# Kernel optimization log

Measured on AMD Instinct MI355X. Metric: run time of the kernel, lower is better.

## Reference

```python
import jax, jax.numpy as jnp
import numpy as np

N, E, F, H, C, T = 100000, 1600000, 128, 64, 8, 4

def setup_inputs() -> dict:
    key = jax.random.key(0)
    ks = jax.random.split(key, 16)
    inp = {
        'x': jax.random.normal(ks[0], (N, F), dtype=jnp.float32),
        'node_types': jax.random.randint(ks[1], (N,), 0, T, dtype=jnp.int64),
        'edge_index0': jax.random.randint(ks[2], (2, E), 0, N, dtype=jnp.int64),
        'edge_index1': jax.random.randint(ks[3], (2, E), 0, N, dtype=jnp.int64),
        # per-node-type input projections
        'W_in': jax.random.normal(ks[4], (T, F, H), dtype=jnp.float32) / np.sqrt(F),
        'b_in': jnp.zeros((T, H), dtype=jnp.float32),
        # 4 GCN convs (layer0: paths [0,0],[0,1]; layer1: paths [0,0],[1,0])
        'W_conv': jax.random.normal(ks[5], (4, H, H), dtype=jnp.float32) / np.sqrt(H),
        'b_conv': jnp.zeros((4, H), dtype=jnp.float32),
        # output attention/classifier layers
        'W1': jax.random.normal(ks[6], (H, H), dtype=jnp.float32) / np.sqrt(H),
        'b1': jnp.zeros((H,), dtype=jnp.float32),
        'W2': jax.random.normal(ks[7], (H, 1), dtype=jnp.float32) / np.sqrt(H),
        'b2': jnp.zeros((1,), dtype=jnp.float32),
        'W3': jax.random.normal(ks[8], (H, C), dtype=jnp.float32) / np.sqrt(H),
        'b3': jnp.zeros((C,), dtype=jnp.float32),
    }
    return inp


def gcn_conv(x, edge_index, W, b):
    # PyG GCNConv: add self-loops, symmetric normalization, then scatter-add.
    n = x.shape[0]
    loop = jnp.arange(n, dtype=edge_index.dtype)
    src = jnp.concatenate([edge_index[0], loop])
    dst = jnp.concatenate([edge_index[1], loop])
    deg = jax.ops.segment_sum(jnp.ones_like(dst, dtype=x.dtype), dst, num_segments=n)
    dinv = jnp.where(deg > 0, jax.lax.rsqrt(deg), 0.0)
    norm = dinv[src] * dinv[dst]            # [E+N]
    xw = x @ W                              # [N,H]
    msg = xw[src] * norm[:, None]           # [E+N,H]
    out = jax.ops.segment_sum(msg, dst, num_segments=n)
    return out + b


def reference(x, node_types, edge_index0, edge_index1,
              W_in, b_in, W_conv, b_conv, W1, b1, W2, b2, W3, b3):
    # per-node-type input linear (fixed small loop over T types)
    hid = jnp.zeros((x.shape[0], H), dtype=x.dtype)
    for t in range(T):
        ht = x @ W_in[t] + b_in[t]
        hid = jnp.where((node_types == t)[:, None], ht, hid)
    edges = [edge_index0, edge_index1]
    states = [hid]
    # layer 0: paths [state 0, adj 0], [state 0, adj 1]; layer_agg = max
    h0 = gcn_conv(states[0], edges[0], W_conv[0], b_conv[0])
    h1 = gcn_conv(states[0], edges[1], W_conv[1], b_conv[1])
    states.append(jnp.maximum(h0, h1))
    # layer 1: paths [state 0, adj 0], [state 1, adj 0]
    h2 = gcn_conv(states[0], edges[0], W_conv[2], b_conv[2])
    h3 = gcn_conv(states[1], edges[0], W_conv[3], b_conv[3])
    states.append(jnp.maximum(h2, h3))
    # LayerNorm (no affine) + gelu (torch default = exact erf form)
    tmp = states[-1]
    mu = jnp.mean(tmp, axis=-1, keepdims=True)
    var = jnp.mean(jnp.square(tmp - mu), axis=-1, keepdims=True)
    tmp = (tmp - mu) * jax.lax.rsqrt(var + 1e-5)
    hidi = jax.nn.gelu(tmp, approximate=False)
    # attention combine over (single) temp state
    attn = jax.nn.softmax(jnp.tanh(hidi @ W1 + b1) @ W2 + b2, axis=-1)  # [N,1] -> ones
    out = attn * hidi
    return out @ W3 + b3
```

## Files before the change

### kernel.cpp

```cpp
#include <hip/hip_runtime.h>
#include <hip/hip_bf16.h>
#include <math.h>


#define HID   64
#define RB    128
#define CHUNK 4096

__device__ __forceinline__ float bflo(unsigned u) { return __int_as_float((int)(u << 16)); }
__device__ __forceinline__ float bfhi(unsigned u) { return __int_as_float((int)(u & 0xFFFF0000u)); }
__device__ __forceinline__ float bf2f(ushort v) { return __int_as_float((int)(((unsigned)v) << 16)); }
__device__ __forceinline__ ushort f2bf(float f) {
    unsigned u = __float_as_uint(f);
    unsigned r = u + 0x7FFFu + ((u >> 16) & 1u);
    return (ushort)(r >> 16);
}

__global__ void zeroRow(unsigned* __restrict__ ghz, unsigned* __restrict__ s1z,
                        float* __restrict__ dinv0, float* __restrict__ dinv1, int N) {
    int tid = threadIdx.x;
    if (tid < 32) { ghz[tid] = 0u; s1z[tid] = 0u; }
    if (tid == 0) { dinv0[N] = 0.0f; dinv1[N] = 0.0f; }
}

__global__ void histA(const int* __restrict__ dst0, const int* __restrict__ dst1,
                      int E, unsigned M, int* __restrict__ bcnt) {
    __shared__ int h[2 * RB];
    for (int i = threadIdx.x; i < 2 * RB; i += blockDim.x) h[i] = 0;
    __syncthreads();
    int stride = gridDim.x * blockDim.x;
    for (int i = blockIdx.x * blockDim.x + threadIdx.x; i < E; i += stride) {
        atomicAdd(&h[__umulhi((unsigned)dst0[i], M)], 1);
        atomicAdd(&h[RB + __umulhi((unsigned)dst1[i], M)], 1);
    }
    __syncthreads();
    for (int i = threadIdx.x; i < 2 * RB; i += blockDim.x)
        if (h[i]) atomicAdd(&bcnt[i], h[i]);
}

__global__ void scanA(const int* __restrict__ bcnt, int* __restrict__ bbase,
                      int* __restrict__ bcur) {
    __shared__ int t[2 * RB];
    int tid = threadIdx.x;
    int orig = bcnt[tid];
    t[tid] = orig;
    __syncthreads();
    int list = tid >> 7, r = tid & (RB - 1);
    for (int o = 1; o < RB; o <<= 1) {
        int u = (r >= o) ? t[tid - o] : 0;
        __syncthreads();
        t[tid] += u;
        __syncthreads();
    }
    int incl = t[tid];
    int excl = incl - orig;
    bbase[list * (RB + 1) + r] = excl;
    bcur[tid] = excl;
    if (r == RB - 1) bbase[list * (RB + 1) + RB] = incl;
}

__global__ void __launch_bounds__(256) partB(const int* __restrict__ e0,
                                             const int* __restrict__ e1,
                                             int E, int BW, unsigned M,
                                             int* __restrict__ bcur_all,
                                             unsigned* __restrict__ arena_all) {
    __shared__ int hist[RB], scn[RB], lbase[RB], cur[RB], gbase[RB];
    __shared__ uint2 buf[CHUNK];
    int half = gridDim.x >> 1;
    int list = (blockIdx.x >= half) ? 1 : 0;
    const int* src = list ? e1 : e0;
    const int* dst = src + E;
    int* bcur = bcur_all + list * RB;
    unsigned* arena = arena_all + (size_t)list * E;
    int blk = blockIdx.x - list * half;
    int tid = threadIdx.x;

    for (int c0 = blk * CHUNK; c0 < E; c0 += half * CHUNK) {
        int cn = min(CHUNK, E - c0);
        for (int i = tid; i < RB; i += 256) hist[i] = 0;
        __syncthreads();
        unsigned ls[16], ld[16];
        #pragma unroll
        for (int k = 0; k < 16; ++k) {
            int j = k * 256 + tid;
            ld[k] = 0xFFFFFFFFu; ls[k] = 0;
            if (j < cn) {
                ls[k] = (unsigned)src[c0 + j];
                ld[k] = (unsigned)dst[c0 + j];
                atomicAdd(&hist[__umulhi(ld[k], M)], 1);
            }
        }
        __syncthreads();
        if (tid < RB) scn[tid] = hist[tid];
        __syncthreads();
        for (int o = 1; o < RB; o <<= 1) {
            int u = (tid < RB && tid >= o) ? scn[tid - o] : 0;
            __syncthreads();
            if (tid < RB) scn[tid] += u;
            __syncthreads();
        }
        if (tid < RB) {
            int ex = scn[tid] - hist[tid];
            lbase[tid] = ex;
            cur[tid]   = ex;
            gbase[tid] = hist[tid] ? atomicAdd(&bcur[tid], hist[tid]) : 0;
        }
        __syncthreads();
        #pragma unroll
        for (int k = 0; k < 16; ++k) {
            if (ld[k] != 0xFFFFFFFFu) {
                int b = __umulhi(ld[k], M);
                int slot = atomicAdd(&cur[b], 1);
                buf[slot] = make_uint2(ls[k], ld[k]);
            }
        }
        __syncthreads();
        for (int i = tid; i < cn; i += 256) {
            uint2 p = buf[i];
            int b = __umulhi(p.y, M);
            arena[gbase[b] + (i - lbase[b])] = (p.x << 10) | (p.y - (unsigned)(b * BW));
        }
        __syncthreads();
    }
}

__global__ void __launch_bounds__(1024) buildC(const unsigned* __restrict__ arena_all,
                                               const int* __restrict__ bbase,
                                               int E, int N, int BW,
                                               int* __restrict__ csr0p, int* __restrict__ csr1p,
                                               unsigned* __restrict__ offp0, unsigned* __restrict__ offp1,
                                               float* __restrict__ dinv0, float* __restrict__ dinv1) {
    __shared__ int degl[800], scn[800], cur[800];
    int list = blockIdx.x >> 7, rb = blockIdx.x & (RB - 1);
    const unsigned* arena = arena_all + (size_t)list * E;
    int* csr = list ? csr1p : csr0p;
    unsigned* offp = list ? offp1 : offp0;
    float* dinv = list ? dinv1 : dinv0;
    int base = bbase[list * (RB + 1) + rb];
    int end  = bbase[list * (RB + 1) + rb + 1];
    int csrb = base + 8 * BW * rb;
    int nbase = rb * BW;
    int nn = min(BW, N - nbase);
    if (nn <= 0) return;
    int tid = threadIdx.x;
    for (int i = tid; i < nn; i += 1024) degl[i] = 0;
    __syncthreads();
    for (int j = base + tid; j < end; j += 1024)
        atomicAdd(&degl[arena[j] & 1023u], 1);
    __syncthreads();
    int d = (tid < nn) ? degl[tid] : 0;
    int dp = d ? ((d + 7) & ~7) : 0;
    if (tid < nn) scn[tid] = dp;
    __syncthreads();
    for (int o = 1; o < nn; o <<= 1) {
        int u = (tid < nn && tid >= o) ? scn[tid - o] : 0;
        __syncthreads();
        if (tid < nn) scn[tid] += u;
        __syncthreads();
    }
    if (tid < nn) {
        int ex = scn[tid] - dp;
        cur[tid] = ex;
        offp[nbase + tid] = (unsigned)(csrb + ex) | ((unsigned)(dp >> 3) << 25);
        dinv[nbase + tid] = rsqrtf((float)(d + 1));
        for (int j = ex + d; j < ex + dp; ++j) csr[csrb + j] = N;
    }
    __syncthreads();
    for (int j = base + tid; j < end; j += 1024) {
        unsigned p = arena[j];
        int loc = atomicAdd(&cur[p & 1023u], 1);
        csr[csrb + loc] = (int)(p >> 10);
    }
}

__global__ void input_proj(const float* __restrict__ x, const int* __restrict__ types,
                           const float* __restrict__ W_in, const float* __restrict__ b_in,
                           ushort* __restrict__ gh, int N, int F) {
    __shared__ float xs[4 * 128];
    int tid = threadIdx.x;
    int w = tid >> 6, h = tid & 63;
    int n0 = blockIdx.x * 4;
    for (int i = tid; i < 4 * F; i += 256) {
        int nn = n0 + i / F;
        xs[i] = (nn < N) ? x[(size_t)nn * F + (i % F)] : 0.0f;
    }
    __syncthreads();
    int n = n0 + w;
    if (n >= N) return;
    int t = types[n];
    const float* W = W_in + (size_t)t * F * HID;
    float acc = b_in[t * HID + h];
    const float* xr = xs + w * F;
    #pragma unroll 4
    for (int f = 0; f < F; ++f)
        acc = fmaf(xr[f], W[(size_t)f * HID + h], acc);
    gh[(size_t)n * HID + h] = f2bf(acc);
}

__device__ __forceinline__ void gather_w(const uint2* __restrict__ GH,
                                         const float* __restrict__ dv,
                                         const int* __restrict__ csr,
                                         unsigned wword, int q, int fl, float a[4]) {
    int base = (int)(wword & 0x1FFFFFFu);
    int it = (int)(wword >> 25);
    if (it == 0) return;
    const int* cp = csr + base;
    int ia = cp[q], ib = cp[4 + q];
    while (true) {
        uint2 va = GH[(size_t)ia * 16 + fl];
        uint2 vb = GH[(size_t)ib * 16 + fl];
        float wa = dv[ia], wb = dv[ib];
        --it; cp += 8;
        int na = 0, nb = 0;
        if (it > 0) { na = cp[q]; nb = cp[4 + q]; }
        a[0] = fmaf(bflo(va.x), wa, a[0]);
        a[1] = fmaf(bfhi(va.x), wa, a[1]);
        a[2] = fmaf(bflo(va.y), wa, a[2]);
        a[3] = fmaf(bfhi(va.y), wa, a[3]);
        a[0] = fmaf(bflo(vb.x), wb, a[0]);
        a[1] = fmaf(bfhi(vb.x), wb, a[1]);
        a[2] = fmaf(bflo(vb.y), wb, a[2]);
        a[3] = fmaf(bfhi(vb.y), wb, a[3]);
        if (it == 0) break;
        ia = na; ib = nb;
    }
}

__device__ __forceinline__ void gather_u(const uint2* __restrict__ GH,
                                         const int* __restrict__ csr,
                                         unsigned wword, int q, int fl, float a[4]) {
    int base = (int)(wword & 0x1FFFFFFu);
    int it = (int)(wword >> 25);
    if (it == 0) return;
    const int* cp = csr + base;
    int ia = cp[q], ib = cp[4 + q];
    while (true) {
        uint2 va = GH[(size_t)ia * 16 + fl];
        uint2 vb = GH[(size_t)ib * 16 + fl];
        --it; cp += 8;
        int na = 0, nb = 0;
        if (it > 0) { na = cp[q]; nb = cp[4 + q]; }
        a[0] += bflo(va.x) + bflo(vb.x);
        a[1] += bfhi(va.x) + bfhi(vb.x);
        a[2] += bflo(va.y) + bflo(vb.y);
        a[3] += bfhi(va.y) + bfhi(vb.y);
        if (it == 0) break;
        ia = na; ib = nb;
    }
}

__global__ void __launch_bounds__(512) gatherL1(
        const ushort* __restrict__ gh,
        const unsigned* __restrict__ offp0, const int* __restrict__ csr0p,
        const float* __restrict__ dinv0,
        const unsigned* __restrict__ offp1, const int* __restrict__ csr1p,
        const float* __restrict__ dinv1,
        const float* __restrict__ W_conv, const float* __restrict__ b_conv,
        unsigned* __restrict__ a0g, ushort* __restrict__ s1g, int N) {
    __shared__ ushort Wb[2 * HID * HID];
    __shared__ float l0[8][HID], l1[8][HID];
    int tid = threadIdx.x;
    for (int i = tid; i < 2 * HID * HID; i += 512) Wb[i] = f2bf(W_conv[i]);
    __syncthreads();
    int w = tid >> 6, lane = tid & 63;
    int q = lane >> 4, fl = lane & 15;
    int n = blockIdx.x * 8 + w;
    if (n >= N) return;
    const uint2* GH = (const uint2*)gh;
    float d0 = dinv0[n], d1 = dinv1[n];
    float a0[4] = {0, 0, 0, 0}, a1[4] = {0, 0, 0, 0};
    if (q == 0) {
        uint2 sv = GH[(size_t)n * 16 + fl];
        a0[0] = bflo(sv.x) * d0; a0[1] = bfhi(sv.x) * d0;
        a0[2] = bflo(sv.y) * d0; a0[3] = bfhi(sv.y) * d0;
        a1[0] = bflo(sv.x) * d1; a1[1] = bfhi(sv.x) * d1;
        a1[2] = bflo(sv.y) * d1; a1[3] = bfhi(sv.y) * d1;
    }
    gather_w(GH, dinv0, csr0p, offp0[n], q, fl, a0);
    gather_w(GH, dinv1, csr1p, offp1[n], q, fl, a1);
    #pragma unroll
    for (int k = 0; k < 4; ++k) {
        a0[k] += __shfl_xor(a0[k], 16, 64);
        a0[k] += __shfl_xor(a0[k], 32, 64);
        a1[k] += __shfl_xor(a1[k], 16, 64);
        a1[k] += __shfl_xor(a1[k], 32, 64);
        a0[k] *= d0;
        a1[k] *= d1;
    }
    if (q == 0) {
        *(float4*)&l0[w][fl * 4] = make_float4(a0[0], a0[1], a0[2], a0[3]);
        *(float4*)&l1[w][fl * 4] = make_float4(a1[0], a1[1], a1[2], a1[3]);
        uint2 pk;
        pk.x = (unsigned)f2bf(a0[0]) | ((unsigned)f2bf(a0[1]) << 16);
        pk.y = (unsigned)f2bf(a0[2]) | ((unsigned)f2bf(a0[3]) << 16);
        ((uint2*)a0g)[(size_t)n * 16 + fl] = pk;
    }
    int h = lane;
    float m0 = b_conv[h];
    float m1 = b_conv[HID + h];
    #pragma unroll 8
    for (int k = 0; k < HID; ++k) {
        m0 = fmaf(l0[w][k], bf2f(Wb[k * HID + h]), m0);
        m1 = fmaf(l1[w][k], bf2f(Wb[HID * HID + k * HID + h]), m1);
    }
    s1g[(size_t)n * HID + h] = f2bf(fmaxf(m0, m1) * d0);
}

__global__ void __launch_bounds__(512) gatherL2(
        const unsigned* __restrict__ a0g, const ushort* __restrict__ s1g,
        const unsigned* __restrict__ offp0, const int* __restrict__ csr0p,
        const float* __restrict__ dinv0,
        const float* __restrict__ W_conv, const float* __restrict__ b_conv,
        const float* __restrict__ W3, const float* __restrict__ b3,
        float* __restrict__ out, int N) {
    __shared__ ushort Wb[2 * HID * HID];
    __shared__ float W3s[HID * 8];
    __shared__ float l2[8][HID], l3[8][HID], gs[8][HID];
    int tid = threadIdx.x;
    for (int i = tid; i < 2 * HID * HID; i += 512) Wb[i] = f2bf(W_conv[2 * HID * HID + i]);
    if (tid < HID * 8) W3s[tid] = W3[tid];
    __syncthreads();
    int w = tid >> 6, lane = tid & 63;
    int q = lane >> 4, fl = lane & 15;
    int n = blockIdx.x * 8 + w;
    if (n >= N) return;
    const uint2* S = (const uint2*)s1g;
    float d0 = dinv0[n];
    float a[4] = {0, 0, 0, 0};
    if (q == 0) {
        uint2 sv = S[(size_t)n * 16 + fl];
        a[0] = bflo(sv.x); a[1] = bfhi(sv.x);
        a[2] = bflo(sv.y); a[3] = bfhi(sv.y);
        uint2 av = ((const uint2*)a0g)[(size_t)n * 16 + fl];
        *(float4*)&l2[w][fl * 4] = make_float4(bflo(av.x), bfhi(av.x), bflo(av.y), bfhi(av.y));
    }
    gather_u(S, csr0p, offp0[n], q, fl, a);
    #pragma unroll
    for (int k = 0; k < 4; ++k) {
        a[k] += __shfl_xor(a[k], 16, 64);
        a[k] += __shfl_xor(a[k], 32, 64);
        a[k] *= d0;
    }
    if (q == 0)
        *(float4*)&l3[w][fl * 4] = make_float4(a[0], a[1], a[2], a[3]);
    int h = lane;
    float m2 = b_conv[2 * HID + h];
    float m3 = b_conv[3 * HID + h];
    #pragma unroll 8
    for (int k = 0; k < HID; ++k) {
        m2 = fmaf(l2[w][k], bf2f(Wb[k * HID + h]), m2);
        m3 = fmaf(l3[w][k], bf2f(Wb[HID * HID + k * HID + h]), m3);
    }
    float s2 = fmaxf(m2, m3);
    float sum = s2;
    #pragma unroll
    for (int off = 32; off; off >>= 1) sum += __shfl_xor(sum, off, 64);
    float mu = sum * (1.0f / 64.0f);
    float dv = s2 - mu;
    float v = dv * dv;
    #pragma unroll
    for (int off = 32; off; off >>= 1) v += __shfl_xor(v, off, 64);
    float xn = dv * rsqrtf(v * (1.0f / 64.0f) + 1e-5f);
    float g = 0.5f * xn * (1.0f + erff(xn * 0.70710678118654752f));
    gs[w][h] = g;
    if (h < 8) {
        float acc = b3[h];
        #pragma unroll 8
        for (int k = 0; k < HID; ++k)
            acc = fmaf(gs[w][k], W3s[k * 8 + h], acc);
        out[(size_t)n * 8 + h] = acc;
    }
}

extern "C" void kernel_launch(void* const* d_in, const int* in_sizes, int n_in,
                              void* d_out, int out_size, void* d_ws, size_t ws_size,
                              hipStream_t stream) {
    const float* x          = (const float*)d_in[0];
    const int*   node_types = (const int*)d_in[1];
    const int*   e0         = (const int*)d_in[2];
    const int*   e1         = (const int*)d_in[3];
    const float* W_in       = (const float*)d_in[4];
    const float* b_in       = (const float*)d_in[5];
    const float* W_conv     = (const float*)d_in[6];
    const float* b_conv     = (const float*)d_in[7];
    const float* W3         = (const float*)d_in[12];
    const float* b3         = (const float*)d_in[13];
    float* out = (float*)d_out;

    int N = in_sizes[1];
    int F = in_sizes[0] / N;
    int E = in_sizes[2] / 2;
    int BW = (N + RB - 1) / RB;
    unsigned M = (unsigned)(0x100000000ULL / (unsigned long long)BW) + 1u;
    size_t EP = (size_t)E + 8 * (size_t)BW * RB + 64;

    unsigned* ws32 = (unsigned*)d_ws;
    int*      bcnt  = (int*)ws32;
    int*      bbase = bcnt + 2 * RB;
    int*      bcur  = bbase + 2 * (RB + 1);
    unsigned* offp0 = (unsigned*)(bcur + 2 * RB + 6);
    unsigned* offp1 = offp0 + (N + 1);
    float*    dinv0 = (float*)(offp1 + (N + 1));
    float*    dinv1 = dinv0 + (N + 1);
    int*      csr0p = (int*)(dinv1 + (N + 1));
    int*      csr1p = csr0p + EP;
    ushort*   gh    = (ushort*)(csr1p + EP);
    ushort*   s1g   = gh + (size_t)(N + 1) * HID;
    unsigned* a0g   = (unsigned*)(s1g + (size_t)(N + 1) * HID);
    unsigned* arena = a0g;

    (void)hipMemsetAsync(bcnt, 0, 2 * RB * sizeof(int), stream);
    zeroRow<<<1, 64, 0, stream>>>((unsigned*)(gh + (size_t)N * HID),
                                  (unsigned*)(s1g + (size_t)N * HID), dinv0, dinv1, N);
    histA<<<1024, 256, 0, stream>>>(e0 + E, e1 + E, E, M, bcnt);
    scanA<<<1, 256, 0, stream>>>(bcnt, bbase, bcur);
    partB<<<256, 256, 0, stream>>>(e0, e1, E, BW, M, bcur, arena);
    buildC<<<2 * RB, 1024, 0, stream>>>(arena, bbase, E, N, BW,
                                        csr0p, csr1p, offp0, offp1, dinv0, dinv1);
    input_proj<<<(N + 3) / 4, 256, 0, stream>>>(x, node_types, W_in, b_in, gh, N, F);
    gatherL1<<<(N + 7) / 8, 512, 0, stream>>>(gh, offp0, csr0p, dinv0, offp1, csr1p, dinv1,
                                              W_conv, b_conv, a0g, s1g, N);
    gatherL2<<<(N + 7) / 8, 512, 0, stream>>>(a0g, s1g, offp0, csr0p, dinv0,
                                              W_conv, b_conv, W3, b3, out, N);
}
```

Measured before the change: 518.3 us.

## Split feature rows into half-width planes and separate gathers from matmuls

The 64-wide bf16 node features are stored as two 32-wide planes, and each sparse gather runs twice, once per plane. The goal is a smaller working set per pass so gathered rows stay in L2. The fused gather+matmul kernels are split into gather-only kernels and separate matM1/matM2 kernels that keep the weights in fp32 shared memory. CSR padding grows from 8 to 16 so each wave covers 16 edges per step with 8 lanes per row. The cost is more kernel launches, extra intermediate writes and reads, doubled index reads, and more padding work.

```diff
diff --git a/kernel.cpp b/kernel.cpp
--- a/kernel.cpp
+++ b/kernel.cpp
@@ -15,11 +15,15 @@
     unsigned r = u + 0x7FFFu + ((u >> 16) & 1u);
     return (ushort)(r >> 16);
 }
-
-__global__ void zeroRow(unsigned* __restrict__ ghz, unsigned* __restrict__ s1z,
+__device__ __forceinline__ unsigned pack2(float lo, float hi) {
+    return (unsigned)f2bf(lo) | ((unsigned)f2bf(hi) << 16);
+}
+
+__global__ void zeroRow(unsigned* __restrict__ ghlo_z, unsigned* __restrict__ ghhi_z,
+                        unsigned* __restrict__ s1lo_z, unsigned* __restrict__ s1hi_z,
                         float* __restrict__ dinv0, float* __restrict__ dinv1, int N) {
     int tid = threadIdx.x;
-    if (tid < 32) { ghz[tid] = 0u; s1z[tid] = 0u; }
+    if (tid < 16) { ghlo_z[tid] = 0u; ghhi_z[tid] = 0u; s1lo_z[tid] = 0u; s1hi_z[tid] = 0u; }
     if (tid == 0) { dinv0[N] = 0.0f; dinv1[N] = 0.0f; }
 }
 
@@ -138,7 +142,7 @@
     float* dinv = list ? dinv1 : dinv0;
     int base = bbase[list * (RB + 1) + rb];
     int end  = bbase[list * (RB + 1) + rb + 1];
-    int csrb = base + 8 * BW * rb;
+    int csrb = base + 16 * BW * rb;
     int nbase = rb * BW;
     int nn = min(BW, N - nbase);
     if (nn <= 0) return;
@@ -149,7 +153,7 @@
         atomicAdd(&degl[arena[j] & 1023u], 1);
     __syncthreads();
     int d = (tid < nn) ? degl[tid] : 0;
-    int dp = d ? ((d + 7) & ~7) : 0;
+    int dp = d ? ((d + 15) & ~15) : 0;
     if (tid < nn) scn[tid] = dp;
     __syncthreads();
     for (int o = 1; o < nn; o <<= 1) {
@@ -161,7 +165,7 @@
     if (tid < nn) {
         int ex = scn[tid] - dp;
         cur[tid] = ex;
-        offp[nbase + tid] = (unsigned)(csrb + ex) | ((unsigned)(dp >> 3) << 25);
+        offp[nbase + tid] = (unsigned)(csrb + ex) | ((unsigned)(dp >> 4) << 25);
         dinv[nbase + tid] = rsqrtf((float)(d + 1));
         for (int j = ex + d; j < ex + dp; ++j) csr[csrb + j] = N;
     }
@@ -175,7 +179,8 @@
 
 __global__ void input_proj(const float* __restrict__ x, const int* __restrict__ types,
                            const float* __restrict__ W_in, const float* __restrict__ b_in,
-                           ushort* __restrict__ gh, int N, int F) {
+                           ushort* __restrict__ ghlo, ushort* __restrict__ ghhi,
+                           int N, int F) {
     __shared__ float xs[4 * 128];
     int tid = threadIdx.x;
     int w = tid >> 6, h = tid & 63;
@@ -194,25 +199,26 @@
     #pragma unroll 4
     for (int f = 0; f < F; ++f)
         acc = fmaf(xr[f], W[(size_t)f * HID + h], acc);
-    gh[(size_t)n * HID + h] = f2bf(acc);
-}
-
-__device__ __forceinline__ void gather_w(const uint2* __restrict__ GH,
-                                         const float* __restrict__ dv,
-                                         const int* __restrict__ csr,
-                                         unsigned wword, int q, int fl, float a[4]) {
+    if (h < 32) ghlo[(size_t)n * 32 + h] = f2bf(acc);
+    else        ghhi[(size_t)n * 32 + h - 32] = f2bf(acc);
+}
+
+__device__ __forceinline__ void gatherW(const uint2* __restrict__ GH,
+                                        const float* __restrict__ dv,
+                                        const int* __restrict__ csr,
+                                        unsigned wword, int q, int fl, float a[4]) {
     int base = (int)(wword & 0x1FFFFFFu);
     int it = (int)(wword >> 25);
     if (it == 0) return;
     const int* cp = csr + base;
-    int ia = cp[q], ib = cp[4 + q];
+    int ia = cp[q], ib = cp[8 + q];
     while (true) {
-        uint2 va = GH[(size_t)ia * 16 + fl];
-        uint2 vb = GH[(size_t)ib * 16 + fl];
+        uint2 va = GH[(size_t)ia * 8 + fl];
+        uint2 vb = GH[(size_t)ib * 8 + fl];
         float wa = dv[ia], wb = dv[ib];
-        --it; cp += 8;
+        --it; cp += 16;
         int na = 0, nb = 0;
-        if (it > 0) { na = cp[q]; nb = cp[4 + q]; }
+        if (it > 0) { na = cp[q]; nb = cp[8 + q]; }
         a[0] = fmaf(bflo(va.x), wa, a[0]);
         a[1] = fmaf(bfhi(va.x), wa, a[1]);
         a[2] = fmaf(bflo(va.y), wa, a[2]);
@@ -226,20 +232,20 @@
     }
 }
 
-__device__ __forceinline__ void gather_u(const uint2* __restrict__ GH,
-                                         const int* __restrict__ csr,
-                                         unsigned wword, int q, int fl, float a[4]) {
+__device__ __forceinline__ void gatherU(const uint2* __restrict__ GH,
+                                        const int* __restrict__ csr,
+                                        unsigned wword, int q, int fl, float a[4]) {
     int base = (int)(wword & 0x1FFFFFFu);
     int it = (int)(wword >> 25);
     if (it == 0) return;
     const int* cp = csr + base;
-    int ia = cp[q], ib = cp[4 + q];
+    int ia = cp[q], ib = cp[8 + q];
     while (true) {
-        uint2 va = GH[(size_t)ia * 16 + fl];
-        uint2 vb = GH[(size_t)ib * 16 + fl];
-        --it; cp += 8;
+        uint2 va = GH[(size_t)ia * 8 + fl];
+        uint2 vb = GH[(size_t)ib * 8 + fl];
+        --it; cp += 16;
         int na = 0, nb = 0;
-        if (it > 0) { na = cp[q]; nb = cp[4 + q]; }
+        if (it > 0) { na = cp[q]; nb = cp[8 + q]; }
         a[0] += bflo(va.x) + bflo(vb.x);
         a[1] += bfhi(va.x) + bfhi(vb.x);
         a[2] += bflo(va.y) + bflo(vb.y);
@@ -249,107 +255,135 @@
     }
 }
 
-__global__ void __launch_bounds__(512) gatherL1(
-        const ushort* __restrict__ gh,
+__global__ void __launch_bounds__(256) gatherG1(
+        const ushort* __restrict__ ghx,
         const unsigned* __restrict__ offp0, const int* __restrict__ csr0p,
         const float* __restrict__ dinv0,
         const unsigned* __restrict__ offp1, const int* __restrict__ csr1p,
         const float* __restrict__ dinv1,
-        const float* __restrict__ W_conv, const float* __restrict__ b_conv,
-        unsigned* __restrict__ a0g, ushort* __restrict__ s1g, int N) {
-    __shared__ ushort Wb[2 * HID * HID];
-    __shared__ float l0[8][HID], l1[8][HID];
-    int tid = threadIdx.x;
-    for (int i = tid; i < 2 * HID * HID; i += 512) Wb[i] = f2bf(W_conv[i]);
-    __syncthreads();
+        ushort* __restrict__ a0out, ushort* __restrict__ a1out, int N) {
+    int tid = threadIdx.x;
     int w = tid >> 6, lane = tid & 63;
-    int q = lane >> 4, fl = lane & 15;
-    int n = blockIdx.x * 8 + w;
+    int q = lane >> 3, fl = lane & 7;
+    int n = blockIdx.x * 4 + w;
     if (n >= N) return;
-    const uint2* GH = (const uint2*)gh;
+    const uint2* GH = (const uint2*)ghx;
     float d0 = dinv0[n], d1 = dinv1[n];
     float a0[4] = {0, 0, 0, 0}, a1[4] = {0, 0, 0, 0};
     if (q == 0) {
-        uint2 sv = GH[(size_t)n * 16 + fl];
-        a0[0] = bflo(sv.x) * d0; a0[1] = bfhi(sv.x) * d0;
-        a0[2] = bflo(sv.y) * d0; a0[3] = bfhi(sv.y) * d0;
-        a1[0] = bflo(sv.x) * d1; a1[1] = bfhi(sv.x) * d1;
-        a1[2] = bflo(sv.y) * d1; a1[3] = bfhi(sv.y) * d1;
-    }
-    gather_w(GH, dinv0, csr0p, offp0[n], q, fl, a0);
-    gather_w(GH, dinv1, csr1p, offp1[n], q, fl, a1);
+        uint2 sv = GH[(size_t)n * 8 + fl];
+        float f0 = bflo(sv.x), f1 = bfhi(sv.x), f2 = bflo(sv.y), f3 = bfhi(sv.y);
+        a0[0] = f0 * d0; a0[1] = f1 * d0; a0[2] = f2 * d0; a0[3] = f3 * d0;
+        a1[0] = f0 * d1; a1[1] = f1 * d1; a1[2] = f2 * d1; a1[3] = f3 * d1;
+    }
+    gatherW(GH, dinv0, csr0p, offp0[n], q, fl, a0);
+    gatherW(GH, dinv1, csr1p, offp1[n], q, fl, a1);
     #pragma unroll
     for (int k = 0; k < 4; ++k) {
+        a0[k] += __shfl_xor(a0[k], 8, 64);
         a0[k] += __shfl_xor(a0[k], 16, 64);
         a0[k] += __shfl_xor(a0[k], 32, 64);
+        a1[k] += __shfl_xor(a1[k], 8, 64);
         a1[k] += __shfl_xor(a1[k], 16, 64);
         a1[k] += __shfl_xor(a1[k], 32, 64);
         a0[k] *= d0;
         a1[k] *= d1;
     }
     if (q == 0) {
-        *(float4*)&l0[w][fl * 4] = make_float4(a0[0], a0[1], a0[2], a0[3]);
-        *(float4*)&l1[w][fl * 4] = make_float4(a1[0], a1[1], a1[2], a1[3]);
-        uint2 pk;
-        pk.x = (unsigned)f2bf(a0[0]) | ((unsigned)f2bf(a0[1]) << 16);
-        pk.y = (unsigned)f2bf(a0[2]) | ((unsigned)f2bf(a0[3]) << 16);
-        ((uint2*)a0g)[(size_t)n * 16 + fl] = pk;
-    }
-    int h = lane;
+        uint2 p0, p1;
+        p0.x = pack2(a0[0], a0[1]); p0.y = pack2(a0[2], a0[3]);
+        p1.x = pack2(a1[0], a1[1]); p1.y = pack2(a1[2], a1[3]);
+        ((uint2*)a0out)[(size_t)n * 8 + fl] = p0;
+        ((uint2*)a1out)[(size_t)n * 8 + fl] = p1;
+    }
+}
+
+__global__ void __launch_bounds__(256) gatherG2(
+        const ushort* __restrict__ s1x,
+        const unsigned* __restrict__ offp0, const int* __restrict__ csr0p,
+        const float* __restrict__ dinv0,
+        ushort* __restrict__ bout, int N) {
+    int tid = threadIdx.x;
+    int w = tid >> 6, lane = tid & 63;
+    int q = lane >> 3, fl = lane & 7;
+    int n = blockIdx.x * 4 + w;
+    if (n >= N) return;
+    const uint2* S = (const uint2*)s1x;
+    float d0 = dinv0[n];
+    float a[4] = {0, 0, 0, 0};
+    if (q == 0) {
+        uint2 sv = S[(size_t)n * 8 + fl];
+        a[0] = bflo(sv.x); a[1] = bfhi(sv.x); a[2] = bflo(sv.y); a[3] = bfhi(sv.y);
+    }
+    gatherU(S, csr0p, offp0[n], q, fl, a);
+    #pragma unroll
+    for (int k = 0; k < 4; ++k) {
+        a[k] += __shfl_xor(a[k], 8, 64);
+        a[k] += __shfl_xor(a[k], 16, 64);
+        a[k] += __shfl_xor(a[k], 32, 64);
+        a[k] *= d0;
+    }
+    if (q == 0) {
+        uint2 p;
+        p.x = pack2(a[0], a[1]); p.y = pack2(a[2], a[3]);
+        ((uint2*)bout)[(size_t)n * 8 + fl] = p;
+    }
+}
+
+__global__ void __launch_bounds__(512) matM1(
+        const ushort* __restrict__ alo0, const ushort* __restrict__ ahi0,
+        const ushort* __restrict__ alo1, const ushort* __restrict__ ahi1,
+        const float* __restrict__ dinv0,
+        const float* __restrict__ W_conv, const float* __restrict__ b_conv,
+        ushort* __restrict__ s1lo, ushort* __restrict__ s1hi, int N) {
+    __shared__ float Ws[2 * HID * HID];
+    __shared__ float ag0[8][HID], ag1[8][HID];
+    int tid = threadIdx.x;
+    for (int i = tid; i < 2 * HID * HID; i += 512) Ws[i] = W_conv[i];
+    __syncthreads();
+    int w = tid >> 6, h = tid & 63;
+    int n = blockIdx.x * 8 + w;
+    if (n >= N) return;
+    float f0 = bf2f(h < 32 ? alo0[(size_t)n * 32 + h] : ahi0[(size_t)n * 32 + h - 32]);
+    float f1 = bf2f(h < 32 ? alo1[(size_t)n * 32 + h] : ahi1[(size_t)n * 32 + h - 32]);
+    ag0[w][h] = f0;
+    ag1[w][h] = f1;
     float m0 = b_conv[h];
     float m1 = b_conv[HID + h];
     #pragma unroll 8
     for (int k = 0; k < HID; ++k) {
-        m0 = fmaf(l0[w][k], bf2f(Wb[k * HID + h]), m0);
-        m1 = fmaf(l1[w][k], bf2f(Wb[HID * HID + k * HID + h]), m1);
-    }
-    s1g[(size_t)n * HID + h] = f2bf(fmaxf(m0, m1) * d0);
-}
-
-__global__ void __launch_bounds__(512) gatherL2(
-        const unsigned* __restrict__ a0g, const ushort* __restrict__ s1g,
-        const unsigned* __restrict__ offp0, const int* __restrict__ csr0p,
-        const float* __restrict__ dinv0,
+        m0 = fmaf(ag0[w][k], Ws[k * HID + h], m0);
+        m1 = fmaf(ag1[w][k], Ws[HID * HID + k * HID + h], m1);
+    }
+    float s1 = fmaxf(m0, m1) * dinv0[n];
+    if (h < 32) s1lo[(size_t)n * 32 + h] = f2bf(s1);
+    else        s1hi[(size_t)n * 32 + h - 32] = f2bf(s1);
+}
+
+__global__ void __launch_bounds__(512) matM2(
+        const ushort* __restrict__ alo0, const ushort* __restrict__ ahi0,
+        const ushort* __restrict__ blo, const ushort* __restrict__ bhi,
         const float* __restrict__ W_conv, const float* __restrict__ b_conv,
         const float* __restrict__ W3, const float* __restrict__ b3,
         float* __restrict__ out, int N) {
-    __shared__ ushort Wb[2 * HID * HID];
+    __shared__ float Ws[2 * HID * HID];
     __shared__ float W3s[HID * 8];
-    __shared__ float l2[8][HID], l3[8][HID], gs[8][HID];
-    int tid = threadIdx.x;
-    for (int i = tid; i < 2 * HID * HID; i += 512) Wb[i] = f2bf(W_conv[2 * HID * HID + i]);
+    __shared__ float ag[8][HID], bg[8][HID], gs[8][HID];
+    int tid = threadIdx.x;
+    for (int i = tid; i < 2 * HID * HID; i += 512) Ws[i] = W_conv[2 * HID * HID + i];
     if (tid < HID * 8) W3s[tid] = W3[tid];
     __syncthreads();
-    int w = tid >> 6, lane = tid & 63;
-    int q = lane >> 4, fl = lane & 15;
+    int w = tid >> 6, h = tid & 63;
     int n = blockIdx.x * 8 + w;
     if (n >= N) return;
-    const uint2* S = (const uint2*)s1g;
-    float d0 = dinv0[n];
-    float a[4] = {0, 0, 0, 0};
-    if (q == 0) {
-        uint2 sv = S[(size_t)n * 16 + fl];
-        a[0] = bflo(sv.x); a[1] = bfhi(sv.x);
-        a[2] = bflo(sv.y); a[3] = bfhi(sv.y);
-        uint2 av = ((const uint2*)a0g)[(size_t)n * 16 + fl];
-        *(float4*)&l2[w][fl * 4] = make_float4(bflo(av.x), bfhi(av.x), bflo(av.y), bfhi(av.y));
-    }
-    gather_u(S, csr0p, offp0[n], q, fl, a);
-    #pragma unroll
-    for (int k = 0; k < 4; ++k) {
-        a[k] += __shfl_xor(a[k], 16, 64);
-        a[k] += __shfl_xor(a[k], 32, 64);
-        a[k] *= d0;
-    }
-    if (q == 0)
-        *(float4*)&l3[w][fl * 4] = make_float4(a[0], a[1], a[2], a[3]);
-    int h = lane;
+    ag[w][h] = bf2f(h < 32 ? alo0[(size_t)n * 32 + h] : ahi0[(size_t)n * 32 + h - 32]);
+    bg[w][h] = bf2f(h < 32 ? blo[(size_t)n * 32 + h] : bhi[(size_t)n * 32 + h - 32]);
     float m2 = b_conv[2 * HID + h];
     float m3 = b_conv[3 * HID + h];
     #pragma unroll 8
     for (int k = 0; k < HID; ++k) {
-        m2 = fmaf(l2[w][k], bf2f(Wb[k * HID + h]), m2);
-        m3 = fmaf(l3[w][k], bf2f(Wb[HID * HID + k * HID + h]), m3);
+        m2 = fmaf(ag[w][k], Ws[k * HID + h], m2);
+        m3 = fmaf(bg[w][k], Ws[HID * HID + k * HID + h], m3);
     }
     float s2 = fmaxf(m2, m3);
     float sum = s2;
@@ -392,7 +426,7 @@
     int E = in_sizes[2] / 2;
     int BW = (N + RB - 1) / RB;
     unsigned M = (unsigned)(0x100000000ULL / (unsigned long long)BW) + 1u;
-    size_t EP = (size_t)E + 8 * (size_t)BW * RB + 64;
+    size_t EP = (size_t)E + 16 * (size_t)BW * RB + 64;
 
     unsigned* ws32 = (unsigned*)d_ws;
     int*      bcnt  = (int*)ws32;
@@ -404,22 +438,39 @@
     float*    dinv1 = dinv0 + (N + 1);
     int*      csr0p = (int*)(dinv1 + (N + 1));
     int*      csr1p = csr0p + EP;
-    ushort*   gh    = (ushort*)(csr1p + EP);
-    ushort*   s1g   = gh + (size_t)(N + 1) * HID;
-    unsigned* a0g   = (unsigned*)(s1g + (size_t)(N + 1) * HID);
-    unsigned* arena = a0g;
+    ushort*   ghlo  = (ushort*)(csr1p + EP);
+    ushort*   ghhi  = ghlo + (size_t)(N + 1) * 32;
+    ushort*   s1lo  = ghhi + (size_t)(N + 1) * 32;
+    ushort*   s1hi  = s1lo + (size_t)(N + 1) * 32;
+    ushort*   alo0  = s1hi + (size_t)(N + 1) * 32;
+    ushort*   ahi0  = alo0 + (size_t)N * 32;
+    ushort*   alo1  = ahi0 + (size_t)N * 32;
+    ushort*   ahi1  = alo1 + (size_t)N * 32;
+    ushort*   blo   = ahi1 + (size_t)N * 32;
+    ushort*   bhi   = blo + (size_t)N * 32;
+    unsigned* arena = (unsigned*)alo0;
 
     (void)hipMemsetAsync(bcnt, 0, 2 * RB * sizeof(int), stream);
-    zeroRow<<<1, 64, 0, stream>>>((unsigned*)(gh + (size_t)N * HID),
-                                  (unsigned*)(s1g + (size_t)N * HID), dinv0, dinv1, N);
+    zeroRow<<<1, 64, 0, stream>>>((unsigned*)(ghlo + (size_t)N * 32),
+                                  (unsigned*)(ghhi + (size_t)N * 32),
+                                  (unsigned*)(s1lo + (size_t)N * 32),
+                                  (unsigned*)(s1hi + (size_t)N * 32),
+                                  dinv0, dinv1, N);
     histA<<<1024, 256, 0, stream>>>(e0 + E, e1 + E, E, M, bcnt);
     scanA<<<1, 256, 0, stream>>>(bcnt, bbase, bcur);
     partB<<<256, 256, 0, stream>>>(e0, e1, E, BW, M, bcur, arena);
     buildC<<<2 * RB, 1024, 0, stream>>>(arena, bbase, E, N, BW,
                                         csr0p, csr1p, offp0, offp1, dinv0, dinv1);
-    input_proj<<<(N + 3) / 4, 256, 0, stream>>>(x, node_types, W_in, b_in, gh, N, F);
-    gatherL1<<<(N + 7) / 8, 512, 0, stream>>>(gh, offp0, csr0p, dinv0, offp1, csr1p, dinv1,
-                                              W_conv, b_conv, a0g, s1g, N);
-    gatherL2<<<(N + 7) / 8, 512, 0, stream>>>(a0g, s1g, offp0, csr0p, dinv0,
-                                              W_conv, b_conv, W3, b3, out, N);
-}
+    input_proj<<<(N + 3) / 4, 256, 0, stream>>>(x, node_types, W_in, b_in,
+                                                ghlo, ghhi, N, F);
+    gatherG1<<<(N + 3) / 4, 256, 0, stream>>>(ghlo, offp0, csr0p, dinv0,
+                                              offp1, csr1p, dinv1, alo0, alo1, N);
+    gatherG1<<<(N + 3) / 4, 256, 0, stream>>>(ghhi, offp0, csr0p, dinv0,
+                                              offp1, csr1p, dinv1, ahi0, ahi1, N);
+    matM1<<<(N + 7) / 8, 512, 0, stream>>>(alo0, ahi0, alo1, ahi1, dinv0,
+                                           W_conv, b_conv, s1lo, s1hi, N);
+    gatherG2<<<(N + 3) / 4, 256, 0, stream>>>(s1lo, offp0, csr0p, dinv0, blo, N);
+    gatherG2<<<(N + 3) / 4, 256, 0, stream>>>(s1hi, offp0, csr0p, dinv0, bhi, N);
+    matM2<<<(N + 7) / 8, 512, 0, stream>>>(alo0, ahi0, blo, bhi,
+                                           W_conv, b_conv, W3, b3, out, N);
+}
```

New measurement: 634.8 us. 1.22x slower.
